# Kernel tuning notes

Measured on AMD Instinct MI355X. Metric: run time of the kernel, lower is better.

## Reference

```python
import jax, jax.numpy as jnp
import numpy as np

EPS = 1e-5
NHEAD = 8

def layer_norm(x, g, b):
    mu = jnp.mean(x, axis=-1, keepdims=True)
    var = jnp.mean((x - mu) ** 2, axis=-1, keepdims=True)
    return (x - mu) * jax.lax.rsqrt(var + EPS) * g + b

def setup_inputs() -> dict:
    key = jax.random.key(0)
    ks = jax.random.split(key, 8)
    B, S, D, F = 4, 2048, 512, 2048
    s = 0.02
    return {
        "x": jax.random.normal(ks[0], (B, S, D), jnp.float32),
        "Wqkv": jax.random.normal(ks[1], (3 * D, D), jnp.float32) * s,
        "bqkv": jnp.zeros((3 * D,), jnp.float32),
        "Wo": jax.random.normal(ks[2], (D, D), jnp.float32) * s,
        "bo": jnp.zeros((D,), jnp.float32),
        "W1": jax.random.normal(ks[3], (F, D), jnp.float32) * s,
        "b1": jnp.zeros((F,), jnp.float32),
        "W2": jax.random.normal(ks[4], (D, F), jnp.float32) * s,
        "b2": jnp.zeros((D,), jnp.float32),
        "g1": jnp.ones((D,), jnp.float32),
        "bn1": jnp.zeros((D,), jnp.float32),
        "g2": jnp.ones((D,), jnp.float32),
        "bn2": jnp.zeros((D,), jnp.float32),
    }

def reference(x, Wqkv, bqkv, Wo, bo, W1, b1, W2, b2, g1, bn1, g2, bn2):
    B, S, D = x.shape
    H = NHEAD
    hd = D // H
    # fused QKV projection (torch MultiheadAttention in_proj)
    qkv = x @ Wqkv.T + bqkv                      # [B,S,3D]
    q, k, v = jnp.split(qkv, 3, axis=-1)
    q = q.reshape(B, S, H, hd).transpose(0, 2, 1, 3)  # [B,H,S,hd]
    k = k.reshape(B, S, H, hd).transpose(0, 2, 1, 3)
    v = v.reshape(B, S, H, hd).transpose(0, 2, 1, 3)
    scores = jnp.einsum("bhqd,bhkd->bhqk", q, k) / jnp.sqrt(jnp.float32(hd))
    causal = jnp.tril(jnp.ones((S, S), bool))
    scores = jnp.where(causal, scores, jnp.float32(-jnp.inf))
    attn = jax.nn.softmax(scores, axis=-1)
    ctx = jnp.einsum("bhqk,bhkd->bhqd", attn, v)        # [B,H,S,hd]
    ctx = ctx.transpose(0, 2, 1, 3).reshape(B, S, D)
    attn_out = ctx @ Wo.T + bo
    # residual + LayerNorm 1
    x = layer_norm(x + attn_out, g1, bn1)
    # FFN (ReLU) + residual + LayerNorm 2
    ff = jax.nn.relu(x @ W1.T + b1) @ W2.T + b2
    x = layer_norm(x + ff, g2, bn2)
    return x
```

## Files before the change

### kernel.cpp

```cpp
#include <hip/hip_runtime.h>
#include <hip/hip_bf16.h>
#include <math.h>

#define D_MODEL 512
#define SEQ     2048
#define BATCH   4
#define NHEADS  8
#define HDIM    64
#define FFN     2048
#define TOKENS  (BATCH*SEQ)

typedef __attribute__((ext_vector_type(8))) short bf16x8;
typedef __attribute__((ext_vector_type(4))) float f32x4;
typedef __attribute__((ext_vector_type(4))) unsigned u32x4;

__device__ inline ushort f2bf(float f) {
    unsigned u = __builtin_bit_cast(unsigned, f);
    unsigned r = (u + 0x7fffu + ((u >> 16) & 1u)) >> 16;
    return (ushort)r;
}

#define GLOAD_LDS16(g, l) __builtin_amdgcn_global_load_lds( \
    (const __attribute__((address_space(1))) void*)(g), \
    (__attribute__((address_space(3))) void*)(l), 16, 0, 0)

__global__ void cast_all_bf16(const float* __restrict__ x, const float* __restrict__ Wqkv,
                              const float* __restrict__ Wo, const float* __restrict__ W1,
                              const float* __restrict__ W2, ushort* __restrict__ outbase) {
    const int i = blockIdx.x * blockDim.x + threadIdx.x;
    if (i >= 1835008) return;
    float4 v;
    if      (i < 1048576) v = ((const float4*)x)[i];
    else if (i < 1245184) v = ((const float4*)Wqkv)[i - 1048576];
    else if (i < 1310720) v = ((const float4*)Wo)[i - 1245184];
    else if (i < 1572864) v = ((const float4*)W1)[i - 1310720];
    else                  v = ((const float4*)W2)[i - 1572864];
    ushort4 o;
    o.x = f2bf(v.x); o.y = f2bf(v.y); o.z = f2bf(v.z); o.w = f2bf(v.w);
    ((ushort4*)outbase)[i] = o;
}

template<int MODE, int RELU>
__global__ __launch_bounds__(256) void gemm_bt_mfma(const ushort* __restrict__ A,
                                                    const ushort* __restrict__ W,
                                                    const float* __restrict__ bias,
                                                    void* __restrict__ CoutA,
                                                    void* __restrict__ CoutB,
                                                    ushort* __restrict__ Qc,
                                                    ushort* __restrict__ Kc,
                                                    ushort* __restrict__ Vt,
                                                    int M, int N, int Kstride, int Klen) {
    __shared__ ushort Asb[2][128 * 32];
    __shared__ ushort Bsb[2][128 * 32];

    const int tid  = threadIdx.x;
    const int lane = tid & 63;
    const int wv   = tid >> 6;
    const int m0   = blockIdx.y * 128;
    const int n0   = blockIdx.x * 128;
    const int wm   = (wv >> 1) * 64;
    const int wn   = (wv & 1) * 64;
    const int ksel = (MODE == 3) ? blockIdx.z : 0;

    const ushort* Ab = A + (size_t)ksel * Klen;
    const ushort* Wb = W + (size_t)ksel * Klen;

    const int rA = wv * 32 + (lane >> 2);
    const int cS = (((lane & 3) ^ ((lane >> 3) & 3)) * 8);
    const ushort* gA0 = Ab + (size_t)(m0 + rA) * Kstride + cS;
    const ushort* gA1 = gA0 + (size_t)16 * Kstride;
    const ushort* gB0 = Wb + (size_t)(n0 + rA) * Kstride + cS;
    const ushort* gB1 = gB0 + (size_t)16 * Kstride;

    f32x4 acc[4][4] = {};

    const int fr  = lane & 15;
    const int fks = (((lane >> 4) ^ ((fr >> 1) & 3)) * 8);

#define STAGE(buf) do { \
        GLOAD_LDS16(gA0, &Asb[buf][wv * 1024]); \
        GLOAD_LDS16(gA1, &Asb[buf][wv * 1024 + 512]); \
        GLOAD_LDS16(gB0, &Bsb[buf][wv * 1024]); \
        GLOAD_LDS16(gB1, &Bsb[buf][wv * 1024 + 512]); \
        gA0 += 32; gA1 += 32; gB0 += 32; gB1 += 32; } while (0)

#define COMPUTE(buf) do { \
        bf16x8 af_[4], bf_[4]; \
        _Pragma("unroll") \
        for (int i_ = 0; i_ < 4; ++i_) \
            af_[i_] = *(const bf16x8*)(&Asb[buf][(wm + i_ * 16 + fr) * 32 + fks]); \
        _Pragma("unroll") \
        for (int j_ = 0; j_ < 4; ++j_) \
            bf_[j_] = *(const bf16x8*)(&Bsb[buf][(wn + j_ * 16 + fr) * 32 + fks]); \
        _Pragma("unroll") \
        for (int i_ = 0; i_ < 4; ++i_) \
            _Pragma("unroll") \
            for (int j_ = 0; j_ < 4; ++j_) \
                acc[i_][j_] = __builtin_amdgcn_mfma_f32_16x16x32_bf16(af_[i_], bf_[j_], acc[i_][j_], 0, 0, 0); \
        } while (0)

#define PSYNC do { \
        asm volatile("s_waitcnt vmcnt(0)" ::: "memory"); \
        __builtin_amdgcn_s_barrier(); \
        __builtin_amdgcn_sched_barrier(0); } while (0)

    STAGE(0);
    PSYNC;
    for (int it = (Klen >> 6) - 1; it > 0; --it) {
        STAGE(1); COMPUTE(0); PSYNC;
        STAGE(0); COMPUTE(1); PSYNC;
    }
    STAGE(1); COMPUTE(0); PSYNC;
    COMPUTE(1);

#undef STAGE
#undef COMPUTE
#undef PSYNC

    const int col  = lane & 15;
    const int rowq = (lane >> 4) * 4;
    #pragma unroll
    for (int i = 0; i < 4; ++i) {
        const int gm = m0 + wm + i * 16 + rowq;
        #pragma unroll
        for (int j = 0; j < 4; ++j) {
            const int gn = n0 + wn + j * 16 + col;
            if (MODE == 2) {
                const float bv = bias[gn];
                const int seg = gn >> 9;
                const int h   = (gn >> 6) & 7;
                const int dd  = gn & 63;
                const int bb  = gm >> 11;
                const int ss  = gm & 2047;
                const int bh  = bb * 8 + h;
                if (seg == 2) {
                    ushort4 pk;
                    pk.x = f2bf(acc[i][j][0] + bv);
                    pk.y = f2bf(acc[i][j][1] + bv);
                    pk.z = f2bf(acc[i][j][2] + bv);
                    pk.w = f2bf(acc[i][j][3] + bv);
                    *(ushort4*)(Vt + ((size_t)bh * 64 + dd) * 2048 + ss) = pk;
                } else {
                    ushort* dst = (seg == 0 ? Qc : Kc) + ((size_t)bh * 2048 + ss) * 64 + dd;
                    #pragma unroll
                    for (int r = 0; r < 4; ++r)
                        dst[(size_t)r * 64] = f2bf(acc[i][j][r] + bv);
                }
            } else if (MODE == 3) {
                float* dst = (float*)(ksel ? CoutB : CoutA);
                const float bv = ksel ? 0.f : bias[gn];
                #pragma unroll
                for (int r = 0; r < 4; ++r)
                    dst[(size_t)(gm + r) * N + gn] = acc[i][j][r] + bv;
            } else {
                const float bv = bias[gn];
                #pragma unroll
                for (int r = 0; r < 4; ++r) {
                    float v = acc[i][j][r] + bv;
                    if (RELU) v = fmaxf(v, 0.f);
                    ((ushort*)CoutA)[(size_t)(gm + r) * N + gn] = f2bf(v);
                }
            }
        }
    }
}

__device__ __forceinline__ void attn_step(const ushort* __restrict__ Kb,
                                          const ushort* __restrict__ Vb,
                                          bf16x8 qf0, bf16x8 qf1,
                                          float& lp, f32x4 (&o)[4],
                                          int qw, int j0, bool diag,
                                          int col, int g, int c7) {
    f32x4 s[4] = {};
    #pragma unroll
    for (int nt = 0; nt < 4; ++nt) {
        const int kr = nt * 16 + col;
        bf16x8 kf0 = *(const bf16x8*)(Kb + kr * 64 + (((g    ) ^ c7) * 8));
        bf16x8 kf1 = *(const bf16x8*)(Kb + kr * 64 + (((g + 4) ^ c7) * 8));
        s[nt] = __builtin_amdgcn_mfma_f32_16x16x32_bf16(kf0, qf0, s[nt], 0, 0, 0);
        s[nt] = __builtin_amdgcn_mfma_f32_16x16x32_bf16(kf1, qf1, s[nt], 0, 0, 0);
    }

    if (diag) {
        #pragma unroll
        for (int nt = 0; nt < 4; ++nt)
            #pragma unroll
            for (int r = 0; r < 4; ++r)
                if ((j0 + nt * 16 + 4 * g + r) > (qw + col)) s[nt][r] = -INFINITY;
    }

    unsigned W[8];
    #pragma unroll
    for (int nt = 0; nt < 4; ++nt) {
        float p0 = __expf(s[nt][0] * 0.125f);
        float p1 = __expf(s[nt][1] * 0.125f);
        float p2 = __expf(s[nt][2] * 0.125f);
        float p3 = __expf(s[nt][3] * 0.125f);
        lp += (p0 + p1) + (p2 + p3);
        asm("v_cvt_pk_bf16_f32 %0, %1, %2" : "=v"(W[2 * nt])     : "v"(p0), "v"(p1));
        asm("v_cvt_pk_bf16_f32 %0, %1, %2" : "=v"(W[2 * nt + 1]) : "v"(p2), "v"(p3));
    }
    asm("v_permlane32_swap_b32 %0, %1" : "+v"(W[0]), "+v"(W[2]));
    asm("v_permlane32_swap_b32 %0, %1" : "+v"(W[1]), "+v"(W[3]));
    asm("v_permlane32_swap_b32 %0, %1" : "+v"(W[4]), "+v"(W[6]));
    asm("v_permlane32_swap_b32 %0, %1" : "+v"(W[5]), "+v"(W[7]));
    asm("v_permlane16_swap_b32 %0, %1" : "+v"(W[0]), "+v"(W[2]));
    asm("v_permlane16_swap_b32 %0, %1" : "+v"(W[1]), "+v"(W[3]));
    asm("v_permlane16_swap_b32 %0, %1" : "+v"(W[4]), "+v"(W[6]));
    asm("v_permlane16_swap_b32 %0, %1" : "+v"(W[5]), "+v"(W[7]));

    u32x4 wa = {W[0], W[1], W[2], W[3]};
    u32x4 wb = {W[4], W[5], W[6], W[7]};
    bf16x8 pf0 = __builtin_bit_cast(bf16x8, wa);
    bf16x8 pf1 = __builtin_bit_cast(bf16x8, wb);

    #pragma unroll
    for (int nt = 0; nt < 4; ++nt) {
        const int vr = nt * 16 + col;
        bf16x8 vf0 = *(const bf16x8*)(Vb + vr * 64 + (((g    ) ^ c7) * 8));
        bf16x8 vf1 = *(const bf16x8*)(Vb + vr * 64 + (((g + 4) ^ c7) * 8));
        o[nt] = __builtin_amdgcn_mfma_f32_16x16x32_bf16(pf0, vf0, o[nt], 0, 0, 0);
        o[nt] = __builtin_amdgcn_mfma_f32_16x16x32_bf16(pf1, vf1, o[nt], 0, 0, 0);
    }
}

__global__ __launch_bounds__(256, 4) void attn_mfma_kernel(const ushort* __restrict__ Qc,
                                                           const ushort* __restrict__ Kc,
                                                           const ushort* __restrict__ Vt,
                                                           ushort* __restrict__ ctxb) {
    __shared__ ushort Ks[2 * 64 * 64];
    __shared__ ushort Vs[2 * 64 * 64];

    const int tid  = threadIdx.x;
    const int lane = tid & 63;
    const int wv   = tid >> 6;
    const int idx  = blockIdx.x;
    const int bh   = (idx & 7) * 4 + (idx >> 7);
    const int pair = (idx >> 3) & 15;
    const int q0a  = pair * 64;
    const int q0b  = (31 - pair) * 64;
    const int qwA  = q0a + wv * 16;
    const int qwB  = q0b + wv * 16;

    const int col = lane & 15;
    const int g   = lane >> 4;
    const int c7  = col & 7;

    bf16x8 qfA0, qfA1, qfB0, qfB1;
    {
        const ushort* qa = Qc + ((size_t)bh * 2048 + qwA + col) * 64 + g * 8;
        qfA0 = *(const bf16x8*)qa;
        qfA1 = *(const bf16x8*)(qa + 32);
        const ushort* qb = Qc + ((size_t)bh * 2048 + qwB + col) * 64 + g * 8;
        qfB0 = *(const bf16x8*)qb;
        qfB1 = *(const bf16x8*)(qb + 32);
    }

    const int srow = tid >> 2;
    const int sch  = 2 * (tid & 3);
    const ushort* Kg = Kc + ((size_t)bh * 2048 + srow) * 64 + sch * 8;
    const ushort* Vg = Vt + ((size_t)bh * 64 + srow) * 2048 + sch * 8;
    const int ko0 = srow * 64 + (((sch    ) ^ (srow & 7)) * 8);
    const int ko1 = srow * 64 + (((sch + 1) ^ (srow & 7)) * 8);

    float lpa = 0.f, lpb = 0.f;
    f32x4 oa[4] = {}, ob[4] = {};

    bf16x8 pk0 = *(const bf16x8*)(Kg);
    bf16x8 pk1 = *(const bf16x8*)(Kg + 8);
    bf16x8 pv0 = *(const bf16x8*)(Vg);
    bf16x8 pv1 = *(const bf16x8*)(Vg + 8);

    for (int j0 = 0; j0 <= q0b; j0 += 64) {
        const int par = (j0 >> 6) & 1;
        ushort* Kb = Ks + par * 4096;
        ushort* Vb = Vs + par * 4096;
        *(bf16x8*)(Kb + ko0) = pk0; *(bf16x8*)(Kb + ko1) = pk1;
        *(bf16x8*)(Vb + ko0) = pv0; *(bf16x8*)(Vb + ko1) = pv1;
        __syncthreads();

        if (j0 < q0b) {
            pk0 = *(const bf16x8*)(Kg + (size_t)(j0 + 64) * 64);
            pk1 = *(const bf16x8*)(Kg + (size_t)(j0 + 64) * 64 + 8);
            pv0 = *(const bf16x8*)(Vg + j0 + 64);
            pv1 = *(const bf16x8*)(Vg + j0 + 72);
        }

        if (j0 <= q0a)
            attn_step(Kb, Vb, qfA0, qfA1, lpa, oa, qwA, j0, j0 == q0a, col, g, c7);
        attn_step(Kb, Vb, qfB0, qfB1, lpb, ob, qwB, j0, j0 == q0b, col, g, c7);
    }

    float la = lpa; la += __shfl_xor(la, 16); la += __shfl_xor(la, 32);
    float lb = lpb; lb += __shfl_xor(lb, 16); lb += __shfl_xor(lb, 32);
    const int b = bh >> 3, h = bh & 7;
    #pragma unroll
    for (int r = 0; r < 4; ++r) {
        const float inva = 1.f / __shfl(la, 4 * g + r);
        const float invb = 1.f / __shfl(lb, 4 * g + r);
        const size_t rowa = ((size_t)b * 2048 + qwA + 4 * g + r) * 512 + h * 64;
        const size_t rowb = ((size_t)b * 2048 + qwB + 4 * g + r) * 512 + h * 64;
        #pragma unroll
        for (int nt = 0; nt < 4; ++nt) {
            ctxb[rowa + nt * 16 + col] = f2bf(oa[nt][r] * inva);
            ctxb[rowb + nt * 16 + col] = f2bf(ob[nt][r] * invb);
        }
    }
}

template<int WRITE_BF16>
__global__ void ln_residual(const float* __restrict__ A, const float* __restrict__ B1,
                            const float* __restrict__ B2,
                            const float* __restrict__ g, const float* __restrict__ beta,
                            float* __restrict__ out, ushort* __restrict__ outb) {
    __shared__ float sbuf[8];
    const int row = blockIdx.x;
    const int tid = threadIdx.x;
    const size_t base = (size_t)row * D_MODEL;

    float v0 = A[base + tid]       + B1[base + tid]       + B2[base + tid];
    float v1 = A[base + tid + 256] + B1[base + tid + 256] + B2[base + tid + 256];

    float sum = v0 + v1;
    #pragma unroll
    for (int off = 32; off; off >>= 1) sum += __shfl_xor(sum, off);
    if ((tid & 63) == 0) sbuf[tid >> 6] = sum;
    __syncthreads();
    if (tid == 0) { float t = 0.f; for (int i = 0; i < 4; ++i) t += sbuf[i]; sbuf[4] = t; }
    __syncthreads();
    const float mu = sbuf[4] * (1.f / 512.f);
    __syncthreads();

    float d0 = v0 - mu, d1 = v1 - mu;
    float sq = d0 * d0 + d1 * d1;
    #pragma unroll
    for (int off = 32; off; off >>= 1) sq += __shfl_xor(sq, off);
    if ((tid & 63) == 0) sbuf[tid >> 6] = sq;
    __syncthreads();
    if (tid == 0) { float t = 0.f; for (int i = 0; i < 4; ++i) t += sbuf[i]; sbuf[4] = t; }
    __syncthreads();
    const float var = sbuf[4] * (1.f / 512.f);
    const float rs  = rsqrtf(var + 1e-5f);

    float r0 = d0 * rs * g[tid]       + beta[tid];
    float r1 = d1 * rs * g[tid + 256] + beta[tid + 256];
    out[base + tid]       = r0;
    out[base + tid + 256] = r1;
    if (WRITE_BF16) {
        outb[base + tid]       = f2bf(r0);
        outb[base + tid + 256] = f2bf(r1);
    }
}

extern "C" void kernel_launch(void* const* d_in, const int* in_sizes, int n_in,
                              void* d_out, int out_size, void* d_ws, size_t ws_size,
                              hipStream_t stream) {
    const float* x    = (const float*)d_in[0];
    const float* Wqkv = (const float*)d_in[1];
    const float* bqkv = (const float*)d_in[2];
    const float* Wo   = (const float*)d_in[3];
    const float* bo   = (const float*)d_in[4];
    const float* W1   = (const float*)d_in[5];
    const float* b1   = (const float*)d_in[6];
    const float* W2   = (const float*)d_in[7];
    const float* b2   = (const float*)d_in[8];
    const float* g1   = (const float*)d_in[9];
    const float* bn1  = (const float*)d_in[10];
    const float* g2   = (const float*)d_in[11];
    const float* bn2  = (const float*)d_in[12];

    float* ws = (float*)d_ws;
    ushort* Qcb     = (ushort*)ws;
    ushort* Kcb     = (ushort*)(ws + 2097152);
    ushort* Vtb     = (ushort*)(ws + 4194304);
    float*  attn_b  = ws;
    ushort* ff1b    = (ushort*)ws;
    float*  ff2a    = ws + 8388608;
    float*  attn_a  = ws + 12582912;
    float*  ff2b    = ws + 12582912;
    float*  ln1     = ws + 16777216;
    ushort* ctxb  = (ushort*)(ws + 20971520);
    ushort* ln1b  = (ushort*)(ws + 23068672);
    ushort* xb    = (ushort*)(ws + 25165824);
    ushort* Wqkvb = (ushort*)(ws + 27262976);
    float*  out   = (float*)d_out;
    ushort* W1b   = (ushort*)(ws + 27787264);
    ushort* W2b   = (ushort*)(ws + 28311552);
    ushort* Wob   = (ushort*)(ws + 27656192);

    const dim3 blk(256);

    cast_all_bf16<<<dim3(7168), blk, 0, stream>>>(x, Wqkv, Wo, W1, W2, xb);

    gemm_bt_mfma<2,0><<<dim3(1536/128, 8192/128), blk, 0, stream>>>(
        xb, Wqkvb, bqkv, nullptr, nullptr, Qcb, Kcb, Vtb, TOKENS, 1536, 512, 512);
    attn_mfma_kernel<<<dim3(512), blk, 0, stream>>>(Qcb, Kcb, Vtb, ctxb);
    gemm_bt_mfma<3,0><<<dim3(512/128, 8192/128, 2), blk, 0, stream>>>(
        ctxb, Wob, bo, attn_a, attn_b, nullptr, nullptr, nullptr, TOKENS, 512, 512, 256);
    ln_residual<1><<<dim3(TOKENS), blk, 0, stream>>>(x, attn_a, attn_b, g1, bn1, ln1, ln1b);
    gemm_bt_mfma<1,1><<<dim3(2048/128, 8192/128), blk, 0, stream>>>(
        ln1b, W1b, b1, ff1b, nullptr, nullptr, nullptr, nullptr, TOKENS, 2048, 512, 512);
    gemm_bt_mfma<3,0><<<dim3(512/128, 8192/128, 2), blk, 0, stream>>>(
        ff1b, W2b, b2, ff2a, ff2b, nullptr, nullptr, nullptr, TOKENS, 512, 2048, 1024);
    ln_residual<0><<<dim3(TOKENS), blk, 0, stream>>>(ln1, ff2a, ff2b, g2, bn2, out, nullptr);
}
```

Measured before the change: 268.8 us.

## Triple-buffer GEMM K-loop and remap block indices for XCD-aware tile placement

Moves the bf16 MFMA GEMM from double to triple LDS buffering. Loads now run two K-tiles ahead, with a partial vmcnt(4) wait in place of a full drain each step, so global-to-LDS traffic overlaps compute more. Block IDs are also remapped so consecutive dispatched blocks (round-robin across 8 XCDs) cover neighbouring M tiles, which should improve L2 reuse. The cost is 50% more LDS per block, and the mapping hardcodes 8 groups of 8 M-tiles, so it assumes a grid of 64 M-tiles.

```diff
diff --git a/kernel.cpp b/kernel.cpp
--- a/kernel.cpp
+++ b/kernel.cpp
@@ -50,14 +50,22 @@
                                                     ushort* __restrict__ Kc,
                                                     ushort* __restrict__ Vt,
                                                     int M, int N, int Kstride, int Klen) {
-    __shared__ ushort Asb[2][128 * 32];
-    __shared__ ushort Bsb[2][128 * 32];
+    __shared__ ushort Asb[3][128 * 32];
+    __shared__ ushort Bsb[3][128 * 32];
 
     const int tid  = threadIdx.x;
     const int lane = tid & 63;
     const int wv   = tid >> 6;
-    const int m0   = blockIdx.y * 128;
-    const int n0   = blockIdx.x * 128;
+
+    const int Gx = gridDim.x;
+    const int f  = blockIdx.x + Gx * blockIdx.y;
+    const int xc = f & 7;
+    const int j  = f >> 3;
+    const int ni = j % Gx;
+    const int mi = xc * 8 + j / Gx;
+    const int m0 = mi * 128;
+    const int n0 = ni * 128;
+
     const int wm   = (wv >> 1) * 64;
     const int wn   = (wv & 1) * 64;
     const int ksel = (MODE == 3) ? blockIdx.z : 0;
@@ -76,22 +84,23 @@
 
     const int fr  = lane & 15;
     const int fks = (((lane >> 4) ^ ((fr >> 1) & 3)) * 8);
-
-#define STAGE(buf) do { \
-        GLOAD_LDS16(gA0, &Asb[buf][wv * 1024]); \
-        GLOAD_LDS16(gA1, &Asb[buf][wv * 1024 + 512]); \
-        GLOAD_LDS16(gB0, &Bsb[buf][wv * 1024]); \
-        GLOAD_LDS16(gB1, &Bsb[buf][wv * 1024 + 512]); \
+    const int lo  = wv * 1024;
+
+#define STAGE(ab, bb) do { \
+        GLOAD_LDS16(gA0, (ab) + lo); \
+        GLOAD_LDS16(gA1, (ab) + lo + 512); \
+        GLOAD_LDS16(gB0, (bb) + lo); \
+        GLOAD_LDS16(gB1, (bb) + lo + 512); \
         gA0 += 32; gA1 += 32; gB0 += 32; gB1 += 32; } while (0)
 
-#define COMPUTE(buf) do { \
+#define COMPUTE(ab, bb) do { \
         bf16x8 af_[4], bf_[4]; \
         _Pragma("unroll") \
         for (int i_ = 0; i_ < 4; ++i_) \
-            af_[i_] = *(const bf16x8*)(&Asb[buf][(wm + i_ * 16 + fr) * 32 + fks]); \
+            af_[i_] = *(const bf16x8*)((ab) + (wm + i_ * 16 + fr) * 32 + fks); \
         _Pragma("unroll") \
         for (int j_ = 0; j_ < 4; ++j_) \
-            bf_[j_] = *(const bf16x8*)(&Bsb[buf][(wn + j_ * 16 + fr) * 32 + fks]); \
+            bf_[j_] = *(const bf16x8*)((bb) + (wn + j_ * 16 + fr) * 32 + fks); \
         _Pragma("unroll") \
         for (int i_ = 0; i_ < 4; ++i_) \
             _Pragma("unroll") \
@@ -99,23 +108,28 @@
                 acc[i_][j_] = __builtin_amdgcn_mfma_f32_16x16x32_bf16(af_[i_], bf_[j_], acc[i_][j_], 0, 0, 0); \
         } while (0)
 
-#define PSYNC do { \
-        asm volatile("s_waitcnt vmcnt(0)" ::: "memory"); \
-        __builtin_amdgcn_s_barrier(); \
-        __builtin_amdgcn_sched_barrier(0); } while (0)
-
-    STAGE(0);
-    PSYNC;
-    for (int it = (Klen >> 6) - 1; it > 0; --it) {
-        STAGE(1); COMPUTE(0); PSYNC;
-        STAGE(0); COMPUTE(1); PSYNC;
-    }
-    STAGE(1); COMPUTE(0); PSYNC;
-    COMPUTE(1);
+    ushort *Ac = Asb[0], *An = Asb[1], *As = Asb[2];
+    ushort *Bc = Bsb[0], *Bn = Bsb[1], *Bs = Bsb[2];
+
+    STAGE(Ac, Bc);
+    STAGE(An, Bn);
+    const int ntiles = Klen >> 5;
+    for (int t = 0; t < ntiles - 1; ++t) {
+        asm volatile("s_waitcnt vmcnt(4)" ::: "memory");
+        __builtin_amdgcn_s_barrier();
+        __builtin_amdgcn_sched_barrier(0);
+        if (t + 2 < ntiles) STAGE(As, Bs);
+        COMPUTE(Ac, Bc);
+        ushort* tA = Ac; Ac = An; An = As; As = tA;
+        ushort* tB = Bc; Bc = Bn; Bn = Bs; Bs = tB;
+    }
+    asm volatile("s_waitcnt vmcnt(0)" ::: "memory");
+    __builtin_amdgcn_s_barrier();
+    __builtin_amdgcn_sched_barrier(0);
+    COMPUTE(Ac, Bc);
 
 #undef STAGE
 #undef COMPUTE
-#undef PSYNC
 
     const int col  = lane & 15;
     const int rowq = (lane >> 4) * 4;
@@ -123,8 +137,8 @@
     for (int i = 0; i < 4; ++i) {
         const int gm = m0 + wm + i * 16 + rowq;
         #pragma unroll
-        for (int j = 0; j < 4; ++j) {
-            const int gn = n0 + wn + j * 16 + col;
+        for (int j2 = 0; j2 < 4; ++j2) {
+            const int gn = n0 + wn + j2 * 16 + col;
             if (MODE == 2) {
                 const float bv = bias[gn];
                 const int seg = gn >> 9;
@@ -135,28 +149,28 @@
                 const int bh  = bb * 8 + h;
                 if (seg == 2) {
                     ushort4 pk;
-                    pk.x = f2bf(acc[i][j][0] + bv);
-                    pk.y = f2bf(acc[i][j][1] + bv);
-                    pk.z = f2bf(acc[i][j][2] + bv);
-                    pk.w = f2bf(acc[i][j][3] + bv);
+                    pk.x = f2bf(acc[i][j2][0] + bv);
+                    pk.y = f2bf(acc[i][j2][1] + bv);
+                    pk.z = f2bf(acc[i][j2][2] + bv);
+                    pk.w = f2bf(acc[i][j2][3] + bv);
                     *(ushort4*)(Vt + ((size_t)bh * 64 + dd) * 2048 + ss) = pk;
                 } else {
                     ushort* dst = (seg == 0 ? Qc : Kc) + ((size_t)bh * 2048 + ss) * 64 + dd;
                     #pragma unroll
                     for (int r = 0; r < 4; ++r)
-                        dst[(size_t)r * 64] = f2bf(acc[i][j][r] + bv);
+                        dst[(size_t)r * 64] = f2bf(acc[i][j2][r] + bv);
                 }
             } else if (MODE == 3) {
                 float* dst = (float*)(ksel ? CoutB : CoutA);
                 const float bv = ksel ? 0.f : bias[gn];
                 #pragma unroll
                 for (int r = 0; r < 4; ++r)
-                    dst[(size_t)(gm + r) * N + gn] = acc[i][j][r] + bv;
+                    dst[(size_t)(gm + r) * N + gn] = acc[i][j2][r] + bv;
             } else {
                 const float bv = bias[gn];
                 #pragma unroll
                 for (int r = 0; r < 4; ++r) {
-                    float v = acc[i][j][r] + bv;
+                    float v = acc[i][j2][r] + bv;
                     if (RELU) v = fmaxf(v, 0.f);
                     ((ushort*)CoutA)[(size_t)(gm + r) * N + gn] = f2bf(v);
                 }
```

Measured after the change: 248.9 us. -7.4%, faster.
